# Optimization experiments

Hardware: AMD Instinct MI355X
Metric: run time of the kernel (lower is better)

Reference implementation:

```python
import jax, jax.numpy as jnp
import numpy as np

H = 16  # num_heads

def _toroidal_bias(S, dtype):
    # float mask: +1.0 at (i, (i-1)%S), (i,i), (i, (i+1)%S); PyTorch ADDS float attn_mask to scores
    eye = jnp.eye(S, dtype=dtype)
    return eye + jnp.roll(eye, 1, axis=1) + jnp.roll(eye, -1, axis=1)

def setup_inputs() -> dict:
    key = jax.random.key(0)
    ks = jax.random.split(key, 7)
    E = 1024
    S, B = 2048, 2
    sc = 0.02
    return {
        "x": jax.random.normal(ks[0], (S, B, E), dtype=jnp.float32),
        "w_tor": jax.random.normal(ks[1], (E, E), dtype=jnp.float32) * sc,
        "b_tor": jax.random.normal(ks[2], (E,), dtype=jnp.float32) * sc,
        "in_proj_w": jax.random.normal(ks[3], (3 * E, E), dtype=jnp.float32) * sc,
        "in_proj_b": jax.random.normal(ks[4], (3 * E,), dtype=jnp.float32) * sc,
        "out_w": jax.random.normal(ks[5], (E, E), dtype=jnp.float32) * sc,
        "out_b": jax.random.normal(ks[6], (E,), dtype=jnp.float32) * sc,
    }

def reference(x, w_tor, b_tor, in_proj_w, in_proj_b, out_w, out_b):
    S, B, E = x.shape
    hd = E // H
    scale = 1.0 / jnp.sqrt(jnp.asarray(hd, dtype=x.dtype))
    # toroidal projection, then fused in_proj (self-attention: q=k=v=x_toroidal)
    xt = x @ w_tor.T + b_tor                      # (S,B,E)
    qkv = xt @ in_proj_w.T + in_proj_b            # (S,B,3E)
    q, k, v = jnp.split(qkv, 3, axis=-1)
    def to_heads(t):
        return t.reshape(S, B, H, hd).transpose(1, 2, 0, 3)  # (B,H,S,hd)
    q, k, v = to_heads(q), to_heads(k), to_heads(v)
    bias = _toroidal_bias(S, x.dtype)             # (S,S) additive float mask
    scores = jnp.einsum('bhqd,bhkd->bhqk', q * scale, k) + bias
    attn = jax.nn.softmax(scores, axis=-1)
    o = jnp.einsum('bhqk,bhkd->bhqd', attn, v)    # (B,H,S,hd)
    o = o.transpose(2, 0, 1, 3).reshape(S, B, E)
    return o @ out_w.T + out_b
```

## Files before the change

### kernel.cpp

```cpp
#include <hip/hip_runtime.h>

#define S_LEN 2048
#define NB    2
#define EMB   1024
#define NH    16
#define HD    64

typedef __bf16 bf16_t;
typedef bf16_t bf16x8 __attribute__((ext_vector_type(8)));
typedef bf16_t bf16x4v __attribute__((ext_vector_type(4)));
typedef float  f32x4  __attribute__((ext_vector_type(4)));
typedef float  f32x16 __attribute__((ext_vector_type(16)));

#define L2E 1.44269504f

__device__ __forceinline__ void g2l16(const void* g, void* l) {
    auto gp = reinterpret_cast<const unsigned int __attribute__((address_space(1)))*>(
        reinterpret_cast<uintptr_t>(g));
    auto lp = reinterpret_cast<unsigned int __attribute__((address_space(3)))*>(
        reinterpret_cast<uintptr_t>(l));
    __builtin_amdgcn_global_load_lds(gp, lp, 16, 0, 0);
}

__device__ __forceinline__ unsigned int pk2(float a, float b) {
    union { unsigned int u; bf16_t h[2]; } r;
    r.h[0] = (bf16_t)a; r.h[1] = (bf16_t)b;
    return r.u;
}

__global__ __launch_bounds__(256) void cast4_f32_bf16(
    const float* __restrict__ s0, bf16_t* __restrict__ d0,
    const float* __restrict__ s1, bf16_t* __restrict__ d1,
    const float* __restrict__ s2, bf16_t* __restrict__ d2,
    const float* __restrict__ s3, bf16_t* __restrict__ d3)
{
    long i = (long)blockIdx.x * 256 + threadIdx.x;
    const float* s; bf16_t* d; long off;
    if (i < 1048576)      { s = s0; d = d0; off = i; }
    else if (i < 1310720) { s = s1; d = d1; off = i - 1048576; }
    else if (i < 2097152) { s = s2; d = d2; off = i - 1310720; }
    else                  { s = s3; d = d3; off = i - 2097152; }
    float4 v = ((const float4*)s)[off];
    bf16x4v o;
    o[0] = (bf16_t)v.x; o[1] = (bf16_t)v.y; o[2] = (bf16_t)v.z; o[3] = (bf16_t)v.w;
    *(bf16x4v*)(d + off * 4) = o;
}

template<int TN, int MODE>
__global__ __launch_bounds__(256) void gemm_bt_bf16(
    const bf16_t* __restrict__ A, const bf16_t* __restrict__ W,
    const float* __restrict__ bias, void* __restrict__ Cout,
    bf16_t* __restrict__ Qp, bf16_t* __restrict__ Kp, bf16_t* __restrict__ Vtp,
    int M, int N, int K)
{
    constexpr int MB = (TN == 128) ? 4 : 2;
    __shared__ __align__(16) bf16_t As[2][128 * 32];
    __shared__ __align__(16) bf16_t Bs[2][TN * 32];

    const int tid  = threadIdx.x;
    const int lane = tid & 63;
    const int w    = tid >> 6;
    const int lm   = lane & 15;
    const int lq   = lane >> 4;
    const long m0  = (long)blockIdx.y * 128;
    const long n0  = (long)blockIdx.x * TN;
    const int wm0  = (TN == 128) ? (w >> 1) * 64 : w * 32;
    const int wn0  = (TN == 128) ? (w & 1) * 64 : 0;

    f32x4 acc[MB][4];
#pragma unroll
    for (int i = 0; i < MB; ++i)
#pragma unroll
        for (int j = 0; j < 4; ++j) acc[i][j] = (f32x4){0.f, 0.f, 0.f, 0.f};

    auto stage = [&](int k0, int buf) {
        bf16_t* asb = &As[buf][0];
        bf16_t* bsb = &Bs[buf][0];
#pragma unroll
        for (int j = 0; j < 2; ++j) {
            int a   = (w * 2 + j) * 64 + lane;
            int row = a >> 2;
            int c   = (a & 3) ^ ((row >> 1) & 3);
            g2l16(A + (m0 + row) * K + k0 + c * 8, asb + (w * 2 + j) * 512);
        }
#pragma unroll
        for (int j = 0; j < TN / 64; ++j) {
            int a   = (w * (TN / 64) + j) * 64 + lane;
            int row = a >> 2;
            int c   = (a & 3) ^ ((row >> 1) & 3);
            g2l16(W + (n0 + row) * K + k0 + c * 8, bsb + (w * (TN / 64) + j) * 512);
        }
    };

    stage(0, 0);
    for (int k0 = 0; k0 < K; k0 += 32) {
        const int cur = (k0 >> 5) & 1;
        asm volatile("s_waitcnt vmcnt(0)" ::: "memory");
        __syncthreads();
        if (k0 + 32 < K) stage(k0 + 32, cur ^ 1);

        bf16x8 af[MB], bfr[4];
#pragma unroll
        for (int mb = 0; mb < MB; ++mb) {
            int r = wm0 + mb * 16 + lm;
            af[mb] = *(const bf16x8*)&As[cur][r * 32 + ((lq ^ ((r >> 1) & 3)) << 3)];
        }
#pragma unroll
        for (int nb = 0; nb < 4; ++nb) {
            int r = wn0 + nb * 16 + lm;
            bfr[nb] = *(const bf16x8*)&Bs[cur][r * 32 + ((lq ^ ((r >> 1) & 3)) << 3)];
        }
#pragma unroll
        for (int mb = 0; mb < MB; ++mb)
#pragma unroll
            for (int nb = 0; nb < 4; ++nb)
                acc[mb][nb] = __builtin_amdgcn_mfma_f32_16x16x32_bf16(
                    af[mb], bfr[nb], acc[mb][nb], 0, 0, 0);
    }

    float b4[4];
#pragma unroll
    for (int nb = 0; nb < 4; ++nb) b4[nb] = bias[n0 + wn0 + nb * 16 + lm];

#pragma unroll
    for (int mb = 0; mb < MB; ++mb) {
#pragma unroll
        for (int r = 0; r < 4; ++r) {
            long m = m0 + wm0 + mb * 16 + lq * 4 + r;
#pragma unroll
            for (int nb = 0; nb < 4; ++nb) {
                int n   = (int)n0 + wn0 + nb * 16 + lm;
                float v = acc[mb][nb][r] + b4[nb];
                if (MODE == 0) {
                    ((float*)Cout)[m * N + n] = v;
                } else if (MODE == 1) {
                    ((bf16_t*)Cout)[m * N + n] = (bf16_t)v;
                } else {
                    int sec  = n >> 10;
                    int nloc = n & 1023;
                    int h    = nloc >> 6;
                    int d    = nloc & 63;
                    int s    = (int)(m >> 1), b = (int)(m & 1);
                    int bh   = b * 16 + h;
                    if (sec == 0) {
                        Qp[((size_t)(bh * S_LEN + s)) * 64 + d] =
                            (bf16_t)(v * (0.125f * L2E));
                    } else if (sec == 1) {
                        Kp[((size_t)(bh * S_LEN + s)) * 64 + d] = (bf16_t)v;
                    } else {
                        Vtp[((size_t)(bh * 64 + d)) * S_LEN + s] = (bf16_t)v;
                    }
                }
            }
        }
    }
}

__global__ __launch_bounds__(256, 2) void attn_mfma(
    const bf16_t* __restrict__ Qb, const bf16_t* __restrict__ Kb,
    const bf16_t* __restrict__ Vtb, bf16_t* __restrict__ O)
{
    __shared__ __align__(16) bf16_t Ks[2][8 * 512];
    __shared__ __align__(16) bf16_t Vts[2][8 * 512];
    __shared__ __align__(16) float  Lw4[4][32];

    const int tid  = threadIdx.x;
    const int lane = tid & 63;
    const int w    = tid >> 6;
    const int wg   = blockIdx.x;
    const int bh   = ((wg & 7) << 2) | (wg >> 7);
    const int qt   = (wg >> 3) & 15;
    const int l5   = lane & 31;
    const int hi   = lane >> 5;

    const bf16_t* qrow = Qb + ((size_t)bh * S_LEN + qt * 128 + w * 32 + l5) * 64 + hi * 8;
    bf16x8 qf[4];
#pragma unroll
    for (int ds = 0; ds < 4; ++ds) qf[ds] = *(const bf16x8*)(qrow + ds * 16);

    f32x16 oacc[2];
#pragma unroll
    for (int dh = 0; dh < 2; ++dh)
#pragma unroll
        for (int i = 0; i < 16; ++i) oacc[dh][i] = 0.f;
    float plsum = 0.f;

    auto stageKV = [&](int kt, int buf) {
        bf16_t* ksb = &Ks[buf][0];
        bf16_t* vsb = &Vts[buf][0];
        const bf16_t* kg = Kb + ((size_t)bh * S_LEN + kt * 64) * 64;
        const bf16_t* vg = Vtb + (size_t)bh * 64 * S_LEN + kt * 64;
#pragma unroll
        for (int j = 0; j < 2; ++j) {
            int c = w * 2 + j;
            g2l16(kg + (size_t)lane * 64 + c * 8,    ksb + c * 512);
            g2l16(vg + (size_t)lane * S_LEN + c * 8, vsb + c * 512);
        }
    };

    stageKV(0, 0);
    for (int kt = 0; kt < 32; ++kt) {
        const int cur = kt & 1;
        asm volatile("s_waitcnt vmcnt(0)" ::: "memory");
        __syncthreads();
        if (kt < 31) stageKV(kt + 1, cur ^ 1);

        f32x16 sacc[2];
        __builtin_amdgcn_s_setprio(1);
#pragma unroll
        for (int kh = 0; kh < 2; ++kh) {
#pragma unroll
            for (int i = 0; i < 16; ++i) sacc[kh][i] = 0.f;
#pragma unroll
            for (int ds = 0; ds < 4; ++ds) {
                bf16x8 kf = *(const bf16x8*)&Ks[cur][(2 * ds + hi) * 512 + (kh * 32 + l5) * 8];
                sacc[kh] = __builtin_amdgcn_mfma_f32_32x32x16_bf16(kf, qf[ds], sacc[kh], 0, 0, 0);
            }
        }
        __builtin_amdgcn_s_setprio(0);

        int ktd = (kt - 2 * qt) & 31;
        if (ktd <= 2 || ktd == 31) {
            int q = qt * 128 + w * 32 + l5;
#pragma unroll
            for (int kh = 0; kh < 2; ++kh)
#pragma unroll
                for (int r = 0; r < 16; ++r) {
                    int key  = kt * 64 + kh * 32 + (r & 3) + 8 * (r >> 2) + 4 * hi;
                    int diff = (key - q) & (S_LEN - 1);
                    if (diff <= 1 || diff == S_LEN - 1) sacc[kh][r] += L2E;
                }
        }

        unsigned int Wp[2][4][2];
#pragma unroll
        for (int kh = 0; kh < 2; ++kh)
#pragma unroll
            for (int g = 0; g < 4; ++g) {
                float p0 = __builtin_amdgcn_exp2f(sacc[kh][g * 4 + 0]);
                float p1 = __builtin_amdgcn_exp2f(sacc[kh][g * 4 + 1]);
                float p2 = __builtin_amdgcn_exp2f(sacc[kh][g * 4 + 2]);
                float p3 = __builtin_amdgcn_exp2f(sacc[kh][g * 4 + 3]);
                plsum += (p0 + p1) + (p2 + p3);
                Wp[kh][g][0] = pk2(p0, p1);
                Wp[kh][g][1] = pk2(p2, p3);
            }

        bf16x8 pf[4];
#pragma unroll
        for (int ks = 0; ks < 4; ++ks) {
            const int kh = ks >> 1, m = ks & 1;
            unsigned int a0 = Wp[kh][2 * m][0],     a1 = Wp[kh][2 * m][1];
            unsigned int b0 = Wp[kh][2 * m + 1][0], b1 = Wp[kh][2 * m + 1][1];
            asm("v_permlane32_swap_b32 %0, %1" : "+v"(a0), "+v"(b0));
            asm("v_permlane32_swap_b32 %0, %1" : "+v"(a1), "+v"(b1));
            union { unsigned int u[4]; bf16x8 v; } cv;
            cv.u[0] = a0; cv.u[1] = a1; cv.u[2] = b0; cv.u[3] = b1;
            pf[ks] = cv.v;
        }

        __builtin_amdgcn_s_setprio(1);
#pragma unroll
        for (int dh = 0; dh < 2; ++dh) {
#pragma unroll
            for (int ks = 0; ks < 4; ++ks) {
                bf16x8 vf = *(const bf16x8*)&Vts[cur][(2 * ks + hi) * 512 + (dh * 32 + l5) * 8];
                oacc[dh] = __builtin_amdgcn_mfma_f32_32x32x16_bf16(pf[ks], vf, oacc[dh], 0, 0, 0);
            }
        }
        __builtin_amdgcn_s_setprio(0);
    }

    plsum += __shfl_xor(plsum, 32, 64);
    if (hi == 0) Lw4[w][l5] = plsum;

    float inv16[16];
#pragma unroll
    for (int g = 0; g < 4; ++g) {
        f32x4 lv = *(const f32x4*)&Lw4[w][8 * g + 4 * hi];
#pragma unroll
        for (int e = 0; e < 4; ++e) inv16[g * 4 + e] = 1.0f / lv[e];
    }

    const int b = bh >> 4, h = bh & 15;
#pragma unroll
    for (int dh = 0; dh < 2; ++dh)
#pragma unroll
        for (int r = 0; r < 16; ++r) {
            int qrel = (r & 3) + 8 * (r >> 2) + 4 * hi;
            int s = qt * 128 + w * 32 + qrel;
            O[((size_t)(s * NB + b)) * EMB + h * 64 + dh * 32 + l5] =
                (bf16_t)(oacc[dh][r] * inv16[r]);
        }
}

extern "C" void kernel_launch(void* const* d_in, const int* in_sizes, int n_in,
                              void* d_out, int out_size, void* d_ws, size_t ws_size,
                              hipStream_t stream)
{
    const float* x         = (const float*)d_in[0];
    const float* w_tor     = (const float*)d_in[1];
    const float* b_tor     = (const float*)d_in[2];
    const float* in_proj_w = (const float*)d_in[3];
    const float* in_proj_b = (const float*)d_in[4];
    const float* out_w     = (const float*)d_in[5];
    const float* out_b     = (const float*)d_in[6];
    float* out = (float*)d_out;

    const int M = S_LEN * NB;

    char* base = (char*)d_ws;
    bf16_t* xb    = (bf16_t*)(base);
    bf16_t* wtorb = (bf16_t*)(base + ( 8ull << 20));
    bf16_t* ipwb  = (bf16_t*)(base + (10ull << 20));
    bf16_t* outwb = (bf16_t*)(base + (16ull << 20));
    bf16_t* xtb   = (bf16_t*)(base + (18ull << 20));
    bf16_t* Kb    = (bf16_t*)(base + (26ull << 20));
    bf16_t* Vtb   = (bf16_t*)(base + (34ull << 20));
    bf16_t* Qb    = xb;
    bf16_t* Ob    = xtb;

    cast4_f32_bf16<<<dim3(9216), 256, 0, stream>>>(
        x, xb, w_tor, wtorb, in_proj_w, ipwb, out_w, outwb);

    gemm_bt_bf16<64, 1><<<dim3(EMB / 64, M / 128), 256, 0, stream>>>(
        xb, wtorb, b_tor, xtb, nullptr, nullptr, nullptr, M, EMB, EMB);

    gemm_bt_bf16<128, 2><<<dim3(3 * EMB / 128, M / 128), 256, 0, stream>>>(
        xtb, ipwb, in_proj_b, nullptr, Qb, Kb, Vtb, M, 3 * EMB, EMB);

    attn_mfma<<<dim3(32 * 16), 256, 0, stream>>>(Qb, Kb, Vtb, Ob);

    gemm_bt_bf16<64, 0><<<dim3(EMB / 64, M / 128), 256, 0, stream>>>(
        Ob, outwb, out_b, out, nullptr, nullptr, nullptr, M, EMB, EMB);
}
```

Measured before the change: 218.5 us.

## Split attention key range across two wave groups per block with LDS reduction

The attention kernel now launches 512 threads per block, and two groups of four waves each process half of the 32 key tiles for the same 128 query rows. Each group keeps its own double-buffered K/V tiles in LDS. At the end, partial row sums and output accumulators are exchanged through shared memory, and each group normalizes and writes one half of the head dimension. This doubles the waves per block to hide latency in the sequential key loop. In exchange it uses about 65 KB of LDS per block, adds a final reduction with extra barriers, and lowers per-wave register headroom.

```diff
diff --git a/kernel.cpp b/kernel.cpp
--- a/kernel.cpp
+++ b/kernel.cpp
@@ -156,24 +156,28 @@
     }
 }
 
-__global__ __launch_bounds__(256, 2) void attn_mfma(
+__global__ __launch_bounds__(512, 4) void attn_mfma(
     const bf16_t* __restrict__ Qb, const bf16_t* __restrict__ Kb,
     const bf16_t* __restrict__ Vtb, bf16_t* __restrict__ O)
 {
-    __shared__ __align__(16) bf16_t Ks[2][8 * 512];
-    __shared__ __align__(16) bf16_t Vts[2][8 * 512];
-    __shared__ __align__(16) float  Lw4[4][32];
+    __shared__ __align__(16) char smem[66560];
+    bf16_t* KsB  = (bf16_t*)smem;
+    bf16_t* VtsB = (bf16_t*)(smem + 32768);
+    float*  Lg   = (float*)(smem + 65536);
+    float*  Xch  = (float*)smem;
 
     const int tid  = threadIdx.x;
     const int lane = tid & 63;
-    const int w    = tid >> 6;
-    const int wg   = blockIdx.x;
-    const int bh   = ((wg & 7) << 2) | (wg >> 7);
-    const int qt   = (wg >> 3) & 15;
+    const int wv   = tid >> 6;
+    const int g    = wv >> 2;
+    const int wq   = wv & 3;
+    const int bid  = blockIdx.x;
+    const int bh   = ((bid & 7) << 2) | (bid >> 7);
+    const int qt   = (bid >> 3) & 15;
     const int l5   = lane & 31;
     const int hi   = lane >> 5;
 
-    const bf16_t* qrow = Qb + ((size_t)bh * S_LEN + qt * 128 + w * 32 + l5) * 64 + hi * 8;
+    const bf16_t* qrow = Qb + ((size_t)bh * S_LEN + qt * 128 + wq * 32 + l5) * 64 + hi * 8;
     bf16x8 qf[4];
 #pragma unroll
     for (int ds = 0; ds < 4; ++ds) qf[ds] = *(const bf16x8*)(qrow + ds * 16);
@@ -185,25 +189,30 @@
         for (int i = 0; i < 16; ++i) oacc[dh][i] = 0.f;
     float plsum = 0.f;
 
-    auto stageKV = [&](int kt, int buf) {
-        bf16_t* ksb = &Ks[buf][0];
-        bf16_t* vsb = &Vts[buf][0];
+    auto stageKV = [&](int t, int buf) {
+        bf16_t* ksb = KsB  + (g * 2 + buf) * 4096;
+        bf16_t* vsb = VtsB + (g * 2 + buf) * 4096;
+        const int kt = g * 16 + t;
         const bf16_t* kg = Kb + ((size_t)bh * S_LEN + kt * 64) * 64;
         const bf16_t* vg = Vtb + (size_t)bh * 64 * S_LEN + kt * 64;
 #pragma unroll
         for (int j = 0; j < 2; ++j) {
-            int c = w * 2 + j;
+            int c = wq * 2 + j;
             g2l16(kg + (size_t)lane * 64 + c * 8,    ksb + c * 512);
             g2l16(vg + (size_t)lane * S_LEN + c * 8, vsb + c * 512);
         }
     };
 
     stageKV(0, 0);
-    for (int kt = 0; kt < 32; ++kt) {
-        const int cur = kt & 1;
+    for (int t = 0; t < 16; ++t) {
+        const int cur = t & 1;
+        const int kt  = g * 16 + t;
         asm volatile("s_waitcnt vmcnt(0)" ::: "memory");
         __syncthreads();
-        if (kt < 31) stageKV(kt + 1, cur ^ 1);
+        if (t < 15) stageKV(t + 1, cur ^ 1);
+
+        const bf16_t* Kc = KsB  + (g * 2 + cur) * 4096;
+        const bf16_t* Vc = VtsB + (g * 2 + cur) * 4096;
 
         f32x16 sacc[2];
         __builtin_amdgcn_s_setprio(1);
@@ -213,7 +222,7 @@
             for (int i = 0; i < 16; ++i) sacc[kh][i] = 0.f;
 #pragma unroll
             for (int ds = 0; ds < 4; ++ds) {
-                bf16x8 kf = *(const bf16x8*)&Ks[cur][(2 * ds + hi) * 512 + (kh * 32 + l5) * 8];
+                bf16x8 kf = *(const bf16x8*)&Kc[(2 * ds + hi) * 512 + (kh * 32 + l5) * 8];
                 sacc[kh] = __builtin_amdgcn_mfma_f32_32x32x16_bf16(kf, qf[ds], sacc[kh], 0, 0, 0);
             }
         }
@@ -221,7 +230,7 @@
 
         int ktd = (kt - 2 * qt) & 31;
         if (ktd <= 2 || ktd == 31) {
-            int q = qt * 128 + w * 32 + l5;
+            int q = qt * 128 + wq * 32 + l5;
 #pragma unroll
             for (int kh = 0; kh < 2; ++kh)
 #pragma unroll
@@ -236,14 +245,14 @@
 #pragma unroll
         for (int kh = 0; kh < 2; ++kh)
 #pragma unroll
-            for (int g = 0; g < 4; ++g) {
-                float p0 = __builtin_amdgcn_exp2f(sacc[kh][g * 4 + 0]);
-                float p1 = __builtin_amdgcn_exp2f(sacc[kh][g * 4 + 1]);
-                float p2 = __builtin_amdgcn_exp2f(sacc[kh][g * 4 + 2]);
-                float p3 = __builtin_amdgcn_exp2f(sacc[kh][g * 4 + 3]);
+            for (int gq = 0; gq < 4; ++gq) {
+                float p0 = __builtin_amdgcn_exp2f(sacc[kh][gq * 4 + 0]);
+                float p1 = __builtin_amdgcn_exp2f(sacc[kh][gq * 4 + 1]);
+                float p2 = __builtin_amdgcn_exp2f(sacc[kh][gq * 4 + 2]);
+                float p3 = __builtin_amdgcn_exp2f(sacc[kh][gq * 4 + 3]);
                 plsum += (p0 + p1) + (p2 + p3);
-                Wp[kh][g][0] = pk2(p0, p1);
-                Wp[kh][g][1] = pk2(p2, p3);
+                Wp[kh][gq][0] = pk2(p0, p1);
+                Wp[kh][gq][1] = pk2(p2, p3);
             }
 
         bf16x8 pf[4];
@@ -264,7 +273,7 @@
         for (int dh = 0; dh < 2; ++dh) {
 #pragma unroll
             for (int ks = 0; ks < 4; ++ks) {
-                bf16x8 vf = *(const bf16x8*)&Vts[cur][(2 * ks + hi) * 512 + (dh * 32 + l5) * 8];
+                bf16x8 vf = *(const bf16x8*)&Vc[(2 * ks + hi) * 512 + (dh * 32 + l5) * 8];
                 oacc[dh] = __builtin_amdgcn_mfma_f32_32x32x16_bf16(pf[ks], vf, oacc[dh], 0, 0, 0);
             }
         }
@@ -272,26 +281,37 @@
     }
 
     plsum += __shfl_xor(plsum, 32, 64);
-    if (hi == 0) Lw4[w][l5] = plsum;
+    if (hi == 0) Lg[(g * 4 + wq) * 32 + l5] = plsum;
+
+    __syncthreads();
+    {
+        float* dst = Xch + g * 4096;
+        const int dhw = 1 - g;
+#pragma unroll
+        for (int r = 0; r < 16; ++r)
+            dst[r * 256 + wq * 64 + lane] = oacc[dhw][r];
+    }
+    __syncthreads();
 
     float inv16[16];
 #pragma unroll
-    for (int g = 0; g < 4; ++g) {
-        f32x4 lv = *(const f32x4*)&Lw4[w][8 * g + 4 * hi];
-#pragma unroll
-        for (int e = 0; e < 4; ++e) inv16[g * 4 + e] = 1.0f / lv[e];
-    }
-
+    for (int g4 = 0; g4 < 4; ++g4) {
+        f32x4 l0 = *(const f32x4*)&Lg[(0 + wq) * 32 + 8 * g4 + 4 * hi];
+        f32x4 l1 = *(const f32x4*)&Lg[(4 + wq) * 32 + 8 * g4 + 4 * hi];
+#pragma unroll
+        for (int e = 0; e < 4; ++e) inv16[g4 * 4 + e] = 1.0f / (l0[e] + l1[e]);
+    }
+
+    const float* src = Xch + (1 - g) * 4096;
     const int b = bh >> 4, h = bh & 15;
 #pragma unroll
-    for (int dh = 0; dh < 2; ++dh)
-#pragma unroll
-        for (int r = 0; r < 16; ++r) {
-            int qrel = (r & 3) + 8 * (r >> 2) + 4 * hi;
-            int s = qt * 128 + w * 32 + qrel;
-            O[((size_t)(s * NB + b)) * EMB + h * 64 + dh * 32 + l5] =
-                (bf16_t)(oacc[dh][r] * inv16[r]);
-        }
+    for (int r = 0; r < 16; ++r) {
+        float v = oacc[g][r] + src[r * 256 + wq * 64 + lane];
+        int qrel = (r & 3) + 8 * (r >> 2) + 4 * hi;
+        int s = qt * 128 + wq * 32 + qrel;
+        O[((size_t)(s * NB + b)) * EMB + h * 64 + g * 32 + l5] =
+            (bf16_t)(v * inv16[r]);
+    }
 }
 
 extern "C" void kernel_launch(void* const* d_in, const int* in_sizes, int n_in,
@@ -329,7 +349,7 @@
     gemm_bt_bf16<128, 2><<<dim3(3 * EMB / 128, M / 128), 256, 0, stream>>>(
         xtb, ipwb, in_proj_b, nullptr, Qb, Kb, Vtb, M, 3 * EMB, EMB);
 
-    attn_mfma<<<dim3(32 * 16), 256, 0, stream>>>(Qb, Kb, Vtb, Ob);
+    attn_mfma<<<dim3(32 * 16), 512, 0, stream>>>(Qb, Kb, Vtb, Ob);
 
     gemm_bt_bf16<64, 0><<<dim3(EMB / 64, M / 128), 256, 0, stream>>>(
         Ob, outwb, out_b, out, nullptr, nullptr, nullptr, M, EMB, EMB);
```

Result: slower. 231.6 us (+6.0%).
